# Kernel tuning notes

Hardware: AMD Instinct MI355X
Metric: run time of the kernel (lower is better)

The kernel has to match this reference:

```python
import jax, jax.numpy as jnp
import numpy as np

B, S, D_IN, D_H = 8, 2048, 1024, 64

def setup_inputs() -> dict:
    key = jax.random.key(0)
    kq, kk, kv, kwq, kwk, kwv = jax.random.split(key, 6)
    sc = 1.0 / np.sqrt(D_IN)
    return {
        "query": jax.random.normal(kq, (B, S, D_IN), dtype=jnp.float32),
        "key": jax.random.normal(kk, (B, S, D_IN), dtype=jnp.float32),
        "value": jax.random.normal(kv, (B, S, D_IN), dtype=jnp.float32),
        # nn.Linear weights: [out, in]
        "W_q": jax.random.normal(kwq, (D_H, D_IN), dtype=jnp.float32) * sc,
        "W_k": jax.random.normal(kwk, (D_H, D_IN), dtype=jnp.float32) * sc,
        "W_v": jax.random.normal(kwv, (D_H, D_IN), dtype=jnp.float32) * sc,
    }

def reference(query, key, value, W_q, W_k, W_v):
    Q = jnp.einsum('bsd,hd->bsh', query, W_q)   # [B,S,D_H]
    K = jnp.einsum('bsd,hd->bsh', key, W_k)
    V = jnp.einsum('bsd,hd->bsh', value, W_v)
    scores = jnp.einsum('bqh,bkh->bqk', Q, K) / jnp.sqrt(jnp.float32(D_H))  # [B,S,S]
    causal = jnp.tril(jnp.ones((S, S), dtype=bool))
    scores = jnp.where(causal, scores, jnp.float32(-jnp.inf))
    attn = jax.nn.softmax(scores, axis=-1)
    return jnp.einsum('bqk,bkh->bqh', attn, V)  # [B,S,D_H]
```

## Files before the change

### kernel.cpp

```cpp
#include <hip/hip_runtime.h>
#include <hip/hip_bf16.h>

#define B_  8
#define S_  2048
#define DIN 1024
#define DH  64

typedef __bf16 bf16;
typedef __attribute__((ext_vector_type(8))) __bf16 bf16x8;
typedef __attribute__((ext_vector_type(4))) float f32x4;

__global__ __launch_bounds__(256) void wconv_kernel(const float* __restrict__ wq,
                                                    const float* __restrict__ wk,
                                                    const float* __restrict__ wv,
                                                    bf16* __restrict__ wb) {
  int i = blockIdx.x * 256 + threadIdx.x;
  int L  = i & 63;
  int kc = (i >> 6) & 31;
  int w  = (i >> 11) & 3;
  int p  = i >> 13;
  const float* src = (p == 0) ? wq : ((p == 1) ? wk : wv);
  int row = w * 16 + (L & 15);
  int k8  = kc * 32 + (L >> 4) * 8;
  const float4* ap = reinterpret_cast<const float4*>(src + (size_t)row * DIN + k8);
  float4 a0 = ap[0], a1 = ap[1];
  bf16x8 av;
  av[0]=(bf16)a0.x; av[1]=(bf16)a0.y; av[2]=(bf16)a0.z; av[3]=(bf16)a0.w;
  av[4]=(bf16)a1.x; av[5]=(bf16)a1.y; av[6]=(bf16)a1.z; av[7]=(bf16)a1.w;
  *reinterpret_cast<bf16x8*>(wb + ((size_t)((p*4 + w)*32 + kc)*64 + L) * 8) = av;
}

__global__ __launch_bounds__(256) void proj_kernel(
    const float* __restrict__ inq, const float* __restrict__ ink, const float* __restrict__ inv,
    const bf16* __restrict__ wb_all,
    bf16* __restrict__ qb, bf16* __restrict__ kb, bf16* __restrict__ vt) {
  const int p = blockIdx.y;
  const float* in = (p == 0) ? inq : ((p == 1) ? ink : inv);
  const int tid  = threadIdx.x;
  const int lane = tid & 63;
  const int w    = tid >> 6;
  const int col16 = lane & 15, g = lane >> 4;
  const int row0 = blockIdx.x * 16;

  __shared__ bf16 albuf[16 * 1024];
  char* alb = (char*)albuf;

  float4 st[16];
  const float* abase = in + (size_t)row0 * DIN;
  #pragma unroll
  for (int c = 0; c < 8; c++) {
    int idx = c * 256 + tid;
    int row = idx >> 7;
    int kk  = (idx & 127) * 8;
    const float4* ap = reinterpret_cast<const float4*>(abase + (size_t)row * DIN + kk);
    st[2*c]   = ap[0];
    st[2*c+1] = ap[1];
  }
  #pragma unroll
  for (int c = 0; c < 8; c++) {
    int idx = c * 256 + tid;
    int row = idx >> 7;
    int kk  = (idx & 127) * 8;
    float4 a0 = st[2*c], a1 = st[2*c+1];
    bf16x8 av;
    av[0]=(bf16)a0.x; av[1]=(bf16)a0.y; av[2]=(bf16)a0.z; av[3]=(bf16)a0.w;
    av[4]=(bf16)a1.x; av[5]=(bf16)a1.y; av[6]=(bf16)a1.z; av[7]=(bf16)a1.w;
    int byte = (row * 2048 + kk * 2) ^ ((row & 7) << 4);
    *reinterpret_cast<bf16x8*>(alb + byte) = av;
  }
  __syncthreads();

  const int wcol = w * 16 + col16;
  const bf16* bbase = wb_all + (size_t)(p*4 + w) * (32 * 64 * 8) + lane * 8;
  f32x4 acc = {};
  #pragma unroll 8
  for (int k0 = 0; k0 < DIN; k0 += 32) {
    int abyte = (col16 * 2048 + (k0 + g * 8) * 2) ^ ((col16 & 7) << 4);
    bf16x8 av = *reinterpret_cast<const bf16x8*>(alb + abyte);
    bf16x8 bv = *reinterpret_cast<const bf16x8*>(bbase + (k0 >> 5) * 512);
    acc = __builtin_amdgcn_mfma_f32_16x16x32_bf16(av, bv, acc, 0, 0, 0);
  }

  #pragma unroll
  for (int rg = 0; rg < 4; rg++) {
    int rr = row0 + g*4 + rg;
    if (p == 0)      qb[(size_t)rr * DH + wcol] = (bf16)acc[rg];
    else if (p == 1) kb[(size_t)rr * DH + wcol] = (bf16)acc[rg];
    else {
      int bb = rr >> 11, ss = rr & 2047;
      vt[((size_t)bb * DH + wcol) * S_ + ss] = (bf16)acc[rg];
    }
  }
}

__global__ __launch_bounds__(512) void attn_kernel(
    const bf16* __restrict__ qb, const bf16* __restrict__ kb, const bf16* __restrict__ vt,
    float* __restrict__ out) {
  const int qt = blockIdx.x;
  const int b  = blockIdx.y;
  const int lane = threadIdx.x & 63;
  const int w    = threadIdx.x >> 6;
  const int col16 = lane & 15, g = lane >> 4;
  const int row0 = qt * 16;

  __shared__ float pacc[8][16][64];
  __shared__ float pm[8][16];
  __shared__ float pl_[8][16];
  __shared__ bf16 plds[8][16 * 64];
  bf16* pl = plds[w];

  bf16x8 qf[2];
  {
    const bf16* qrow = qb + ((size_t)(b * S_ + row0 + col16)) * DH + g * 8;
    qf[0] = *reinterpret_cast<const bf16x8*>(qrow);
    qf[1] = *reinterpret_cast<const bf16x8*>(qrow + 32);
  }

  f32x4 acc[4] = {};
  float m_r[4], l_r[4];
  #pragma unroll
  for (int i = 0; i < 4; i++) { m_r[i] = -1e30f; l_r[i] = 0.f; }

  const int nt = (qt + 4) >> 2;

  for (int t = w; t < nt; t += 8) {
    const int kvb = t * 64;
    f32x4 s[4] = {};
    #pragma unroll
    for (int n = 0; n < 4; n++) {
      const bf16* krow = kb + ((size_t)(b * S_ + kvb + n*16 + col16)) * DH + g * 8;
      bf16x8 kf0 = *reinterpret_cast<const bf16x8*>(krow);
      bf16x8 kf1 = *reinterpret_cast<const bf16x8*>(krow + 32);
      s[n] = __builtin_amdgcn_mfma_f32_16x16x32_bf16(qf[0], kf0, s[n], 0, 0, 0);
      s[n] = __builtin_amdgcn_mfma_f32_16x16x32_bf16(qf[1], kf1, s[n], 0, 0, 0);
    }
    float vals[4][4];
    const bool diag = (t == nt - 1);
    #pragma unroll
    for (int n = 0; n < 4; n++)
      #pragma unroll
      for (int rg = 0; rg < 4; rg++) {
        float v = s[n][rg] * 0.125f;
        if (diag) {
          int kvp = kvb + n*16 + col16;
          int qp  = row0 + g*4 + rg;
          if (kvp > qp) v = -1e30f;
        }
        vals[n][rg] = v;
      }
    float rmax[4];
    #pragma unroll
    for (int rg = 0; rg < 4; rg++)
      rmax[rg] = fmaxf(fmaxf(vals[0][rg], vals[1][rg]), fmaxf(vals[2][rg], vals[3][rg]));
    #pragma unroll
    for (int off = 1; off < 16; off <<= 1)
      #pragma unroll
      for (int rg = 0; rg < 4; rg++)
        rmax[rg] = fmaxf(rmax[rg], __shfl_xor(rmax[rg], off));
    float scl[4], rsum[4];
    #pragma unroll
    for (int rg = 0; rg < 4; rg++) {
      float mn = fmaxf(m_r[rg], rmax[rg]);
      scl[rg] = __expf(m_r[rg] - mn);
      m_r[rg] = mn;
      rsum[rg] = 0.f;
    }
    #pragma unroll
    for (int n = 0; n < 4; n++)
      #pragma unroll
      for (int rg = 0; rg < 4; rg++) {
        float pp = __expf(vals[n][rg] - m_r[rg]);
        vals[n][rg] = pp;
        rsum[rg] += pp;
      }
    #pragma unroll
    for (int off = 1; off < 16; off <<= 1)
      #pragma unroll
      for (int rg = 0; rg < 4; rg++)
        rsum[rg] += __shfl_xor(rsum[rg], off);
    #pragma unroll
    for (int rg = 0; rg < 4; rg++)
      l_r[rg] = l_r[rg] * scl[rg] + rsum[rg];
    #pragma unroll
    for (int n = 0; n < 4; n++)
      #pragma unroll
      for (int rg = 0; rg < 4; rg++)
        acc[n][rg] *= scl[rg];
    #pragma unroll
    for (int n = 0; n < 4; n++)
      #pragma unroll
      for (int rg = 0; rg < 4; rg++) {
        int row = g*4 + rg;
        int idx = (row * 64 + n*16 + col16) ^ ((row & 7) << 3);
        pl[idx] = (bf16)vals[n][rg];
      }
    bf16x8 pa[2];
    {
      int row = col16;
      int i0 = (row * 64 + 0  + g * 8) ^ ((row & 7) << 3);
      int i1 = (row * 64 + 32 + g * 8) ^ ((row & 7) << 3);
      pa[0] = *reinterpret_cast<const bf16x8*>(&pl[i0]);
      pa[1] = *reinterpret_cast<const bf16x8*>(&pl[i1]);
    }
    #pragma unroll
    for (int nd = 0; nd < 4; nd++) {
      const bf16* vrow = vt + ((size_t)(b * DH + nd*16 + col16)) * S_ + kvb + g * 8;
      bf16x8 v0 = *reinterpret_cast<const bf16x8*>(vrow);
      bf16x8 v1 = *reinterpret_cast<const bf16x8*>(vrow + 32);
      acc[nd] = __builtin_amdgcn_mfma_f32_16x16x32_bf16(pa[0], v0, acc[nd], 0, 0, 0);
      acc[nd] = __builtin_amdgcn_mfma_f32_16x16x32_bf16(pa[1], v1, acc[nd], 0, 0, 0);
    }
  }

  #pragma unroll
  for (int n = 0; n < 4; n++)
    #pragma unroll
    for (int rg = 0; rg < 4; rg++)
      pacc[w][g*4 + rg][n*16 + col16] = acc[n][rg];
  if (col16 == 0) {
    #pragma unroll
    for (int rg = 0; rg < 4; rg++) {
      pm[w][g*4 + rg]  = m_r[rg];
      pl_[w][g*4 + rg] = l_r[rg];
    }
  }
  __syncthreads();

  const int tid = threadIdx.x;
  #pragma unroll
  for (int i = 0; i < 2; i++) {
    int idx = tid + i * 512;
    int row = idx >> 6, col = idx & 63;
    float M = -1e30f;
    #pragma unroll
    for (int ww = 0; ww < 8; ww++) M = fmaxf(M, pm[ww][row]);
    float L = 0.f, o = 0.f;
    #pragma unroll
    for (int ww = 0; ww < 8; ww++) {
      float e = __expf(pm[ww][row] - M);
      L += pl_[ww][row] * e;
      o += pacc[ww][row][col] * e;
    }
    out[((size_t)b * S_ + row0 + row) * DH + col] = o / L;
  }
}

extern "C" void kernel_launch(void* const* d_in, const int* in_sizes, int n_in,
                              void* d_out, int out_size, void* d_ws, size_t ws_size,
                              hipStream_t stream) {
  const float* q  = (const float*)d_in[0];
  const float* k  = (const float*)d_in[1];
  const float* v  = (const float*)d_in[2];
  const float* wq = (const float*)d_in[3];
  const float* wk = (const float*)d_in[4];
  const float* wv = (const float*)d_in[5];

  char* ws = (char*)d_ws;
  bf16* Wb = (bf16*)(ws);
  bf16* Qb = (bf16*)(ws + 1572864);
  bf16* Kb = (bf16*)(ws + 1572864 + 2097152);
  bf16* Vt = (bf16*)(ws + 1572864 + 4194304);

  wconv_kernel<<<dim3(96), 256, 0, stream>>>(wq, wk, wv, Wb);
  proj_kernel<<<dim3(B_ * S_ / 16, 3), 256, 0, stream>>>(q, k, v, Wb, Qb, Kb, Vt);
  attn_kernel<<<dim3(S_ / 16, B_), 512, 0, stream>>>(Qb, Kb, Vt, (float*)d_out);
}
```

Baseline: 95.97 us.

## Give each wave its own 16-row tile and drop LDS staging in projection

The projection kernel no longer stages a shared 16-row fp32 A tile through LDS with a block barrier. Each wave now owns a 16-row tile and loads A directly from global memory in MFMA fragment layout, with a two-deep register prefetch. Each wave computes all four 16-column output blocks, so one A fragment feeds four MFMAs and the grid shrinks by 4x. This removes the LDS round trip and the __syncthreads, but each lane's global loads are now 32-byte chunks strided by rows, which may coalesce less well, and weight reads per wave rise fourfold.

```diff
diff --git a/kernel.cpp b/kernel.cpp
--- a/kernel.cpp
+++ b/kernel.cpp
@@ -40,57 +40,50 @@
   const int lane = tid & 63;
   const int w    = tid >> 6;
   const int col16 = lane & 15, g = lane >> 4;
-  const int row0 = blockIdx.x * 16;
-
-  __shared__ bf16 albuf[16 * 1024];
-  char* alb = (char*)albuf;
-
-  float4 st[16];
-  const float* abase = in + (size_t)row0 * DIN;
-  #pragma unroll
-  for (int c = 0; c < 8; c++) {
-    int idx = c * 256 + tid;
-    int row = idx >> 7;
-    int kk  = (idx & 127) * 8;
-    const float4* ap = reinterpret_cast<const float4*>(abase + (size_t)row * DIN + kk);
-    st[2*c]   = ap[0];
-    st[2*c+1] = ap[1];
-  }
-  #pragma unroll
-  for (int c = 0; c < 8; c++) {
-    int idx = c * 256 + tid;
-    int row = idx >> 7;
-    int kk  = (idx & 127) * 8;
-    float4 a0 = st[2*c], a1 = st[2*c+1];
+  const int tile = blockIdx.x * 4 + w;
+  const int row0 = tile * 16;
+
+  const float* arow = in + (size_t)(row0 + col16) * DIN + g * 8;
+  const bf16*  bbase = wb_all + (size_t)p * 4 * 16384 + lane * 8;
+
+  f32x4 acc[4] = {};
+  float4 pf0[2], pf1[2];
+  pf0[0] = *reinterpret_cast<const float4*>(arow);
+  pf1[0] = *reinterpret_cast<const float4*>(arow + 4);
+  pf0[1] = *reinterpret_cast<const float4*>(arow + 32);
+  pf1[1] = *reinterpret_cast<const float4*>(arow + 36);
+
+  #pragma unroll
+  for (int kc = 0; kc < 32; kc++) {
+    float4 a0 = pf0[kc & 1], a1 = pf1[kc & 1];
+    if (kc + 2 < 32) {
+      pf0[kc & 1] = *reinterpret_cast<const float4*>(arow + (kc + 2) * 32);
+      pf1[kc & 1] = *reinterpret_cast<const float4*>(arow + (kc + 2) * 32 + 4);
+    }
     bf16x8 av;
     av[0]=(bf16)a0.x; av[1]=(bf16)a0.y; av[2]=(bf16)a0.z; av[3]=(bf16)a0.w;
     av[4]=(bf16)a1.x; av[5]=(bf16)a1.y; av[6]=(bf16)a1.z; av[7]=(bf16)a1.w;
-    int byte = (row * 2048 + kk * 2) ^ ((row & 7) << 4);
-    *reinterpret_cast<bf16x8*>(alb + byte) = av;
-  }
-  __syncthreads();
-
-  const int wcol = w * 16 + col16;
-  const bf16* bbase = wb_all + (size_t)(p*4 + w) * (32 * 64 * 8) + lane * 8;
-  f32x4 acc = {};
-  #pragma unroll 8
-  for (int k0 = 0; k0 < DIN; k0 += 32) {
-    int abyte = (col16 * 2048 + (k0 + g * 8) * 2) ^ ((col16 & 7) << 4);
-    bf16x8 av = *reinterpret_cast<const bf16x8*>(alb + abyte);
-    bf16x8 bv = *reinterpret_cast<const bf16x8*>(bbase + (k0 >> 5) * 512);
-    acc = __builtin_amdgcn_mfma_f32_16x16x32_bf16(av, bv, acc, 0, 0, 0);
-  }
-
-  #pragma unroll
-  for (int rg = 0; rg < 4; rg++) {
-    int rr = row0 + g*4 + rg;
-    if (p == 0)      qb[(size_t)rr * DH + wcol] = (bf16)acc[rg];
-    else if (p == 1) kb[(size_t)rr * DH + wcol] = (bf16)acc[rg];
-    else {
-      int bb = rr >> 11, ss = rr & 2047;
-      vt[((size_t)bb * DH + wcol) * S_ + ss] = (bf16)acc[rg];
-    }
-  }
+    #pragma unroll
+    for (int n = 0; n < 4; n++) {
+      bf16x8 bv = *reinterpret_cast<const bf16x8*>(bbase + n * 16384 + kc * 512);
+      acc[n] = __builtin_amdgcn_mfma_f32_16x16x32_bf16(av, bv, acc[n], 0, 0, 0);
+    }
+  }
+
+  const int rowbase = row0 + g * 4;
+  #pragma unroll
+  for (int n = 0; n < 4; n++)
+    #pragma unroll
+    for (int rg = 0; rg < 4; rg++) {
+      int rr = rowbase + rg;
+      int cc = n * 16 + col16;
+      if (p == 0)      qb[(size_t)rr * DH + cc] = (bf16)acc[n][rg];
+      else if (p == 1) kb[(size_t)rr * DH + cc] = (bf16)acc[n][rg];
+      else {
+        int bb = rr >> 11, ss = rr & 2047;
+        vt[((size_t)bb * DH + cc) * S_ + ss] = (bf16)acc[n][rg];
+      }
+    }
 }
 
 __global__ __launch_bounds__(512) void attn_kernel(
@@ -262,6 +255,6 @@
   bf16* Vt = (bf16*)(ws + 1572864 + 4194304);
 
   wconv_kernel<<<dim3(96), 256, 0, stream>>>(wq, wk, wv, Wb);
-  proj_kernel<<<dim3(B_ * S_ / 16, 3), 256, 0, stream>>>(q, k, v, Wb, Qb, Kb, Vt);
+  proj_kernel<<<dim3(B_ * S_ / 64, 3), 256, 0, stream>>>(q, k, v, Wb, Qb, Kb, Vt);
   attn_kernel<<<dim3(S_ / 16, B_), 512, 0, stream>>>(Qb, Kb, Vt, (float*)d_out);
 }
```

Result: slower. 98.98 us (+3.1%).
